# Kernel optimization log

Measured on AMD Instinct MI355X. Metric: run time of the kernel, lower is better.

Reference implementation:

```python
import jax, jax.numpy as jnp
import numpy as np

N_NODES = 50000
N_EDGES = 800000
IN_CH, HID_CH, OUT_CH = 128, 256, 128


def setup_inputs() -> dict:
    key = jax.random.key(0)
    k1, k2, k3, k4 = jax.random.split(key, 4)
    x = jax.random.normal(k1, (N_NODES, IN_CH), dtype=jnp.float32)
    edge_index = jax.random.randint(k2, (2, N_EDGES), 0, N_NODES, dtype=jnp.int32)
    # Glorot-ish scaled weights
    W1 = jax.random.normal(k3, (IN_CH, HID_CH), dtype=jnp.float32) * (1.0 / np.sqrt(IN_CH))
    b1 = jnp.zeros((HID_CH,), dtype=jnp.float32)
    W2 = jax.random.normal(k4, (HID_CH, OUT_CH), dtype=jnp.float32) * (1.0 / np.sqrt(HID_CH))
    b2 = jnpp = jnp.zeros((OUT_CH,), dtype=jnp.float32)
    return {"x": x, "edge_index": edge_index, "W1": W1, "b1": b1, "W2": W2, "b2": b2}


def _gcn_conv(x, W, b, src, dst, num_nodes):
    """PyG GCNConv: add self-loops, symmetric deg^-1/2 norm, linear, scatter-add."""
    h = x @ W  # [N, out] dense transform first (as in GCNConv)
    # in-degree including self-loops (edge weights = 1)
    deg = jax.ops.segment_sum(jnp.ones_like(dst, dtype=h.dtype), dst, num_segments=num_nodes)
    deg = deg + 1.0  # self-loop contribution
    dinv = jnp.where(deg > 0, jax.lax.rsqrt(deg), 0.0)
    # neighbor messages: norm_e * h[src_e], scatter-added to dst
    norm = dinv[src] * dinv[dst]                      # [E]
    msg = h[src] * norm[:, None]                      # [E, out] gather
    agg = jax.ops.segment_sum(msg, dst, num_segments=num_nodes)  # scatter-add
    # self-loop messages: dinv[i]^2 * h[i]
    agg = agg + h * (dinv * dinv)[:, None]
    return agg + b


def reference(x, edge_index, W1, b1, W2, b2):
    src, dst = edge_index[0], edge_index[1]
    n = x.shape[0]
    h = jax.nn.relu(_gcn_conv(x, W1, b1, src, dst, n))
    return _gcn_conv(h, W2, b2, src, dst, n)
```

## Files before the change

### kernel.cpp

```cpp
#include <hip/hip_runtime.h>

#define N_NODES 50000
#define N_EDGES 800000
#define IN_CH 128
#define HID_CH 256
#define OUT_CH 128
#define BUCKET 64

#define N_XCD 8
#define NODES_PER_XCD 6250

using half8 = __attribute__((ext_vector_type(8))) _Float16;
using f32x4 = __attribute__((ext_vector_type(4))) float;


#define FILL_CHUNKS 3125
#define FILL_BLOCKS (FILL_CHUNKS * N_XCD)
#define CVT_BLOCKS 3125
#define WT1_BLOCKS 256
#define WT2_BLOCKS 128

__global__ __launch_bounds__(256) void prep_kernel(const int* __restrict__ src,
                                                   const int* __restrict__ dst,
                                                   int* __restrict__ cnt,
                                                   unsigned short* __restrict__ bucket,
                                                   const float* __restrict__ x,
                                                   _Float16* __restrict__ x16,
                                                   const float* __restrict__ W1,
                                                   _Float16* __restrict__ W1T,
                                                   const float* __restrict__ W2,
                                                   _Float16* __restrict__ W2T) {
    int b = blockIdx.x, t = threadIdx.x;
    if (b < FILL_BLOCKS) {
        int g = b & 7;
        int chunk = b >> 3;
        int i = chunk * 256 + t;
        if (i < N_EDGES) {
            int d = dst[i];
            int lo = g * NODES_PER_XCD;
            if (d >= lo && d < lo + NODES_PER_XCD) {
                int s = src[i];
                int p = atomicAdd(&cnt[d], 1);
                if (p < BUCKET) bucket[(size_t)d * BUCKET + p] = (unsigned short)s;
            }
        }
    } else if (b < FILL_BLOCKS + CVT_BLOCKS) {
        int i = (b - FILL_BLOCKS) * 256 + t;
        float4 v0 = ((const float4*)x)[i * 2];
        float4 v1 = ((const float4*)x)[i * 2 + 1];
        half8 o = {(_Float16)v0.x, (_Float16)v0.y, (_Float16)v0.z, (_Float16)v0.w,
                   (_Float16)v1.x, (_Float16)v1.y, (_Float16)v1.z, (_Float16)v1.w};
        ((half8*)x16)[i] = o;
    } else if (b < FILL_BLOCKS + CVT_BLOCKS + WT1_BLOCKS) {
        int n = b - FILL_BLOCKS - CVT_BLOCKS;
        if (t < IN_CH) W1T[(size_t)n * IN_CH + t] = (_Float16)W1[(size_t)t * HID_CH + n];
    } else {
        int n = b - FILL_BLOCKS - CVT_BLOCKS - WT1_BLOCKS;
        if (t < HID_CH) W2T[(size_t)n * HID_CH + t] = (_Float16)W2[(size_t)t * OUT_CH + n];
    }
}


template <bool OUT16>
__global__ __launch_bounds__(256) void agg16_kernel(const _Float16* __restrict__ h16,
                                                    const int* __restrict__ cnt,
                                                    const unsigned short* __restrict__ bucket,
                                                    const float* __restrict__ bias,
                                                    void* __restrict__ outp) {
    int t = blockIdx.x * 256 + threadIdx.x;
    int v = t >> 4;
    int sub = t & 15;
    int deg = min(cnt[v], BUCKET);
    float dv = rsqrtf((float)cnt[v] + 1.0f);
    half8 hv = ((const half8*)(h16 + (size_t)v * 128))[sub];
    float acc[8];
#pragma unroll
    for (int i = 0; i < 8; i++) acc[i] = (float)hv[i] * dv * dv;

    const unsigned short* bk = bucket + (size_t)v * BUCKET;
    for (int base = 0; base < deg; base += 16) {
        int idx = base + sub;
        int a = 0;
        float c = 0.f;
        if (idx < deg) {
            a = bk[idx];
            c = rsqrtf((float)cnt[a] + 1.0f) * dv;
        }
        int len = min(deg - base, 16);
        int j = 0;
        for (; j + 8 <= len; j += 8) {
            int   s0 = __shfl(a, j + 0, 16); float w0 = __shfl(c, j + 0, 16);
            int   s1 = __shfl(a, j + 1, 16); float w1 = __shfl(c, j + 1, 16);
            int   s2 = __shfl(a, j + 2, 16); float w2 = __shfl(c, j + 2, 16);
            int   s3 = __shfl(a, j + 3, 16); float w3 = __shfl(c, j + 3, 16);
            int   s4 = __shfl(a, j + 4, 16); float w4 = __shfl(c, j + 4, 16);
            int   s5 = __shfl(a, j + 5, 16); float w5 = __shfl(c, j + 5, 16);
            int   s6 = __shfl(a, j + 6, 16); float w6 = __shfl(c, j + 6, 16);
            int   s7 = __shfl(a, j + 7, 16); float w7 = __shfl(c, j + 7, 16);
            half8 x0 = ((const half8*)(h16 + (size_t)s0 * 128))[sub];
            half8 x1 = ((const half8*)(h16 + (size_t)s1 * 128))[sub];
            half8 x2 = ((const half8*)(h16 + (size_t)s2 * 128))[sub];
            half8 x3 = ((const half8*)(h16 + (size_t)s3 * 128))[sub];
            half8 x4 = ((const half8*)(h16 + (size_t)s4 * 128))[sub];
            half8 x5 = ((const half8*)(h16 + (size_t)s5 * 128))[sub];
            half8 x6 = ((const half8*)(h16 + (size_t)s6 * 128))[sub];
            half8 x7 = ((const half8*)(h16 + (size_t)s7 * 128))[sub];
#pragma unroll
            for (int i = 0; i < 8; i++) acc[i] += w0 * (float)x0[i];
#pragma unroll
            for (int i = 0; i < 8; i++) acc[i] += w1 * (float)x1[i];
#pragma unroll
            for (int i = 0; i < 8; i++) acc[i] += w2 * (float)x2[i];
#pragma unroll
            for (int i = 0; i < 8; i++) acc[i] += w3 * (float)x3[i];
#pragma unroll
            for (int i = 0; i < 8; i++) acc[i] += w4 * (float)x4[i];
#pragma unroll
            for (int i = 0; i < 8; i++) acc[i] += w5 * (float)x5[i];
#pragma unroll
            for (int i = 0; i < 8; i++) acc[i] += w6 * (float)x6[i];
#pragma unroll
            for (int i = 0; i < 8; i++) acc[i] += w7 * (float)x7[i];
        }
        for (; j + 4 <= len; j += 4) {
            int   s0 = __shfl(a, j + 0, 16); float w0 = __shfl(c, j + 0, 16);
            int   s1 = __shfl(a, j + 1, 16); float w1 = __shfl(c, j + 1, 16);
            int   s2 = __shfl(a, j + 2, 16); float w2 = __shfl(c, j + 2, 16);
            int   s3 = __shfl(a, j + 3, 16); float w3 = __shfl(c, j + 3, 16);
            half8 x0 = ((const half8*)(h16 + (size_t)s0 * 128))[sub];
            half8 x1 = ((const half8*)(h16 + (size_t)s1 * 128))[sub];
            half8 x2 = ((const half8*)(h16 + (size_t)s2 * 128))[sub];
            half8 x3 = ((const half8*)(h16 + (size_t)s3 * 128))[sub];
#pragma unroll
            for (int i = 0; i < 8; i++) acc[i] += w0 * (float)x0[i];
#pragma unroll
            for (int i = 0; i < 8; i++) acc[i] += w1 * (float)x1[i];
#pragma unroll
            for (int i = 0; i < 8; i++) acc[i] += w2 * (float)x2[i];
#pragma unroll
            for (int i = 0; i < 8; i++) acc[i] += w3 * (float)x3[i];
        }
        for (; j < len; j++) {
            int   s = __shfl(a, j, 16);
            float w = __shfl(c, j, 16);
            half8 xv = ((const half8*)(h16 + (size_t)s * 128))[sub];
#pragma unroll
            for (int i = 0; i < 8; i++) acc[i] += w * (float)xv[i];
        }
    }

    if (OUT16) {
        half8 o;
#pragma unroll
        for (int i = 0; i < 8; i++) o[i] = (_Float16)acc[i];
        ((half8*)outp)[(size_t)v * 16 + sub] = o;
    } else {
        const float4* bp = (const float4*)bias;
        float4 b0 = bp[sub * 2], b1v = bp[sub * 2 + 1];
        float4 o0 = make_float4(acc[0] + b0.x, acc[1] + b0.y, acc[2] + b0.z, acc[3] + b0.w);
        float4 o1 = make_float4(acc[4] + b1v.x, acc[5] + b1v.y, acc[6] + b1v.z, acc[7] + b1v.w);
        float4* op = (float4*)outp;
        op[(size_t)v * 32 + sub * 2] = o0;
        op[(size_t)v * 32 + sub * 2 + 1] = o1;
    }
}


__global__ __launch_bounds__(256) void fused_mlp_kernel(const _Float16* __restrict__ A,
                                                        const _Float16* __restrict__ W1T,
                                                        const float* __restrict__ b1,
                                                        const _Float16* __restrict__ W2T,
                                                        _Float16* __restrict__ T2, int M) {
    const int LDH = 264;
    const int LDA = 136;
    const int LDB = 40;
    __shared__ __align__(16) _Float16 h1s[64 * LDH];
    __shared__ __align__(16) _Float16 As[64 * LDA];
    __shared__ __align__(16) _Float16 Bs[128 * LDB];

    int tid = threadIdx.x;
    int wave = tid >> 6, lane = tid & 63;
    int quad = lane >> 4, l16 = lane & 15;
    int wm = wave >> 1, wn = wave & 1;
    int bm = blockIdx.x * 64;

    for (int q = tid; q < 64 * 16; q += 256) {
        int row = q >> 4, seg = q & 15;
        int gr = bm + row;
        float4 v = make_float4(0.f, 0.f, 0.f, 0.f);
        if (gr < M) v = *(const float4*)(A + (size_t)gr * IN_CH + seg * 8);
        *(float4*)(As + row * LDA + seg * 8) = v;
    }

    for (int nh = 0; nh < 2; nh++) {
        f32x4 acc[2][4] = {};
        for (int k0 = 0; k0 < IN_CH; k0 += 32) {
            for (int q = tid; q < 512; q += 256) {
                int row = q >> 2, seg = q & 3;
                float4 v = *(const float4*)(W1T + (size_t)(nh * 128 + row) * IN_CH + k0 + seg * 8);
                *(float4*)(Bs + row * LDB + seg * 8) = v;
            }
            __syncthreads();
            half8 af[2], bf[4];
#pragma unroll
            for (int mt = 0; mt < 2; mt++)
                af[mt] = *(const half8*)(As + (wm * 32 + mt * 16 + l16) * LDA + k0 + quad * 8);
#pragma unroll
            for (int nt = 0; nt < 4; nt++)
                bf[nt] = *(const half8*)(Bs + (wn * 64 + nt * 16 + l16) * LDB + quad * 8);
#pragma unroll
            for (int mt = 0; mt < 2; mt++)
#pragma unroll
                for (int nt = 0; nt < 4; nt++)
                    acc[mt][nt] = __builtin_amdgcn_mfma_f32_16x16x32_f16(af[mt], bf[nt], acc[mt][nt], 0, 0, 0);
            __syncthreads();
        }
#pragma unroll
        for (int mt = 0; mt < 2; mt++)
#pragma unroll
            for (int nt = 0; nt < 4; nt++)
#pragma unroll
                for (int r = 0; r < 4; r++) {
                    int ml = wm * 32 + mt * 16 + quad * 4 + r;
                    int nl = wn * 64 + nt * 16 + l16;
                    float v = acc[mt][nt][r] + b1[nh * 128 + nl];
                    h1s[ml * LDH + nh * 128 + nl] = (_Float16)fmaxf(v, 0.f);
                }
    }

    f32x4 acc2[2][4] = {};
    for (int k0 = 0; k0 < HID_CH; k0 += 32) {
        for (int q = tid; q < 512; q += 256) {
            int row = q >> 2, seg = q & 3;
            float4 v = *(const float4*)(W2T + (size_t)row * HID_CH + k0 + seg * 8);
            *(float4*)(Bs + row * LDB + seg * 8) = v;
        }
        __syncthreads();
        half8 af[2], bf[4];
#pragma unroll
        for (int mt = 0; mt < 2; mt++)
            af[mt] = *(const half8*)(h1s + (wm * 32 + mt * 16 + l16) * LDH + k0 + quad * 8);
#pragma unroll
        for (int nt = 0; nt < 4; nt++)
            bf[nt] = *(const half8*)(Bs + (wn * 64 + nt * 16 + l16) * LDB + quad * 8);
#pragma unroll
        for (int mt = 0; mt < 2; mt++)
#pragma unroll
            for (int nt = 0; nt < 4; nt++)
                acc2[mt][nt] = __builtin_amdgcn_mfma_f32_16x16x32_f16(af[mt], bf[nt], acc2[mt][nt], 0, 0, 0);
        __syncthreads();
    }

    _Float16* Cs = As;
#pragma unroll
    for (int mt = 0; mt < 2; mt++)
#pragma unroll
        for (int nt = 0; nt < 4; nt++)
#pragma unroll
            for (int r = 0; r < 4; r++) {
                int ml = wm * 32 + mt * 16 + quad * 4 + r;
                int nl = wn * 64 + nt * 16 + l16;
                Cs[ml * LDA + nl] = (_Float16)acc2[mt][nt][r];
            }
    __syncthreads();
    for (int q = tid; q < 64 * 16; q += 256) {
        int row = q >> 4, seg = q & 15;
        int gr = bm + row;
        if (gr < M)
            *(float4*)(T2 + (size_t)gr * OUT_CH + seg * 8) = *(const float4*)(Cs + row * LDA + seg * 8);
    }
}


extern "C" void kernel_launch(void* const* d_in, const int* in_sizes, int n_in,
                              void* d_out, int out_size, void* d_ws, size_t ws_size,
                              hipStream_t stream) {
    const float* x  = (const float*)d_in[0];
    const int*   ei = (const int*)d_in[1];
    const int*   src = ei;
    const int*   dst = ei + N_EDGES;
    const float* W1 = (const float*)d_in[2];
    const float* b1 = (const float*)d_in[3];
    const float* W2 = (const float*)d_in[4];
    const float* b2 = (const float*)d_in[5];
    float* out = (float*)d_out;

    char* w = (char*)d_ws;
    auto alloc = [&](size_t bytes) -> void* {
        void* p = (void*)w;
        w += (bytes + 255) & ~(size_t)255;
        return p;
    };
    int*            cnt    = (int*)alloc((size_t)N_NODES * 4);
    unsigned short* bucket = (unsigned short*)alloc((size_t)N_NODES * BUCKET * 2);
    _Float16*       x16    = (_Float16*)alloc((size_t)N_NODES * IN_CH * 2);
    _Float16*       a1     = (_Float16*)alloc((size_t)N_NODES * IN_CH * 2);
    _Float16*       t2     = (_Float16*)alloc((size_t)N_NODES * OUT_CH * 2);
    _Float16*       W1T    = (_Float16*)alloc((size_t)IN_CH * HID_CH * 2);
    _Float16*       W2T    = (_Float16*)alloc((size_t)HID_CH * OUT_CH * 2);

    hipMemsetAsync(cnt, 0, (size_t)N_NODES * 4, stream);

    prep_kernel<<<FILL_BLOCKS + CVT_BLOCKS + WT1_BLOCKS + WT2_BLOCKS, 256, 0, stream>>>(
        src, dst, cnt, bucket, x, x16, W1, W1T, W2, W2T);

    agg16_kernel<true><<<N_NODES * 16 / 256, 256, 0, stream>>>(x16, cnt, bucket, nullptr, a1);
    fused_mlp_kernel<<<(N_NODES + 63) / 64, 256, 0, stream>>>(a1, W1T, b1, W2T, t2, N_NODES);
    agg16_kernel<false><<<N_NODES * 16 / 256, 256, 0, stream>>>(t2, cnt, bucket, b2, out);
}
```

Before: 217.5 us.

## Load MLP operand fragments directly from global memory, drop LDS staging

The fused MLP kernel no longer stages the input tile and weight tiles in shared memory. Each wave reads its A fragments and W1T/W2T fragments straight from global memory (weights come through L2), which removes most __syncthreads barriers. Shared memory use drops to only the hidden buffer, which can allow higher occupancy. The cost is redundant global weight loads across waves and blocks in exchange for fewer barriers and less LDS traffic.

```diff
diff --git a/kernel.cpp b/kernel.cpp
--- a/kernel.cpp
+++ b/kernel.cpp
@@ -172,11 +172,8 @@
                                                         const _Float16* __restrict__ W2T,
                                                         _Float16* __restrict__ T2, int M) {
     const int LDH = 264;
-    const int LDA = 136;
-    const int LDB = 40;
+    const int LDC = 136;
     __shared__ __align__(16) _Float16 h1s[64 * LDH];
-    __shared__ __align__(16) _Float16 As[64 * LDA];
-    __shared__ __align__(16) _Float16 Bs[128 * LDB];
 
     int tid = threadIdx.x;
     int wave = tid >> 6, lane = tid & 63;
@@ -184,74 +181,69 @@
     int wm = wave >> 1, wn = wave & 1;
     int bm = blockIdx.x * 64;
 
-    for (int q = tid; q < 64 * 16; q += 256) {
-        int row = q >> 4, seg = q & 15;
-        int gr = bm + row;
-        float4 v = make_float4(0.f, 0.f, 0.f, 0.f);
-        if (gr < M) v = *(const float4*)(A + (size_t)gr * IN_CH + seg * 8);
-        *(float4*)(As + row * LDA + seg * 8) = v;
-    }
-
+    half8 af[2][4];
+#pragma unroll
+    for (int mt = 0; mt < 2; mt++) {
+        int ar = bm + wm * 32 + mt * 16 + l16;
+        ar = min(ar, M - 1);
+#pragma unroll
+        for (int kq = 0; kq < 4; kq++)
+            af[mt][kq] = *(const half8*)(A + (size_t)ar * IN_CH + kq * 32 + quad * 8);
+    }
+
+#pragma unroll
     for (int nh = 0; nh < 2; nh++) {
         f32x4 acc[2][4] = {};
-        for (int k0 = 0; k0 < IN_CH; k0 += 32) {
-            for (int q = tid; q < 512; q += 256) {
-                int row = q >> 2, seg = q & 3;
-                float4 v = *(const float4*)(W1T + (size_t)(nh * 128 + row) * IN_CH + k0 + seg * 8);
-                *(float4*)(Bs + row * LDB + seg * 8) = v;
+#pragma unroll
+        for (int kq = 0; kq < 4; kq++) {
+            half8 bf[4];
+#pragma unroll
+            for (int nt = 0; nt < 4; nt++) {
+                int br = nh * 128 + wn * 64 + nt * 16 + l16;
+                bf[nt] = *(const half8*)(W1T + (size_t)br * IN_CH + kq * 32 + quad * 8);
             }
-            __syncthreads();
-            half8 af[2], bf[4];
 #pragma unroll
             for (int mt = 0; mt < 2; mt++)
-                af[mt] = *(const half8*)(As + (wm * 32 + mt * 16 + l16) * LDA + k0 + quad * 8);
-#pragma unroll
-            for (int nt = 0; nt < 4; nt++)
-                bf[nt] = *(const half8*)(Bs + (wn * 64 + nt * 16 + l16) * LDB + quad * 8);
+#pragma unroll
+                for (int nt = 0; nt < 4; nt++)
+                    acc[mt][nt] = __builtin_amdgcn_mfma_f32_16x16x32_f16(af[mt][kq], bf[nt], acc[mt][nt], 0, 0, 0);
+        }
+#pragma unroll
+        for (int nt = 0; nt < 4; nt++) {
+            int nl = wn * 64 + nt * 16 + l16;
+            float bb = b1[nh * 128 + nl];
 #pragma unroll
             for (int mt = 0; mt < 2; mt++)
-#pragma unroll
-                for (int nt = 0; nt < 4; nt++)
-                    acc[mt][nt] = __builtin_amdgcn_mfma_f32_16x16x32_f16(af[mt], bf[nt], acc[mt][nt], 0, 0, 0);
-            __syncthreads();
-        }
-#pragma unroll
-        for (int mt = 0; mt < 2; mt++)
-#pragma unroll
-            for (int nt = 0; nt < 4; nt++)
 #pragma unroll
                 for (int r = 0; r < 4; r++) {
                     int ml = wm * 32 + mt * 16 + quad * 4 + r;
-                    int nl = wn * 64 + nt * 16 + l16;
-                    float v = acc[mt][nt][r] + b1[nh * 128 + nl];
-                    h1s[ml * LDH + nh * 128 + nl] = (_Float16)fmaxf(v, 0.f);
+                    h1s[ml * LDH + nh * 128 + nl] = (_Float16)fmaxf(acc[mt][nt][r] + bb, 0.f);
                 }
-    }
+        }
+    }
+    __syncthreads();
 
     f32x4 acc2[2][4] = {};
-    for (int k0 = 0; k0 < HID_CH; k0 += 32) {
-        for (int q = tid; q < 512; q += 256) {
-            int row = q >> 2, seg = q & 3;
-            float4 v = *(const float4*)(W2T + (size_t)row * HID_CH + k0 + seg * 8);
-            *(float4*)(Bs + row * LDB + seg * 8) = v;
-        }
-        __syncthreads();
-        half8 af[2], bf[4];
+#pragma unroll
+    for (int kq = 0; kq < 8; kq++) {
+        half8 a2[2], bf[4];
 #pragma unroll
         for (int mt = 0; mt < 2; mt++)
-            af[mt] = *(const half8*)(h1s + (wm * 32 + mt * 16 + l16) * LDH + k0 + quad * 8);
-#pragma unroll
-        for (int nt = 0; nt < 4; nt++)
-            bf[nt] = *(const half8*)(Bs + (wn * 64 + nt * 16 + l16) * LDB + quad * 8);
+            a2[mt] = *(const half8*)(h1s + (wm * 32 + mt * 16 + l16) * LDH + kq * 32 + quad * 8);
+#pragma unroll
+        for (int nt = 0; nt < 4; nt++) {
+            int br = wn * 64 + nt * 16 + l16;
+            bf[nt] = *(const half8*)(W2T + (size_t)br * HID_CH + kq * 32 + quad * 8);
+        }
 #pragma unroll
         for (int mt = 0; mt < 2; mt++)
 #pragma unroll
             for (int nt = 0; nt < 4; nt++)
-                acc2[mt][nt] = __builtin_amdgcn_mfma_f32_16x16x32_f16(af[mt], bf[nt], acc2[mt][nt], 0, 0, 0);
-        __syncthreads();
-    }
-
-    _Float16* Cs = As;
+                acc2[mt][nt] = __builtin_amdgcn_mfma_f32_16x16x32_f16(a2[mt], bf[nt], acc2[mt][nt], 0, 0, 0);
+    }
+    __syncthreads();
+
+    _Float16* Cs = h1s;
 #pragma unroll
     for (int mt = 0; mt < 2; mt++)
 #pragma unroll
@@ -260,14 +252,14 @@
             for (int r = 0; r < 4; r++) {
                 int ml = wm * 32 + mt * 16 + quad * 4 + r;
                 int nl = wn * 64 + nt * 16 + l16;
-                Cs[ml * LDA + nl] = (_Float16)acc2[mt][nt][r];
+                Cs[ml * LDC + nl] = (_Float16)acc2[mt][nt][r];
             }
     __syncthreads();
     for (int q = tid; q < 64 * 16; q += 256) {
         int row = q >> 4, seg = q & 15;
         int gr = bm + row;
         if (gr < M)
-            *(float4*)(T2 + (size_t)gr * OUT_CH + seg * 8) = *(const float4*)(Cs + row * LDA + seg * 8);
+            *(float4*)(T2 + (size_t)gr * OUT_CH + seg * 8) = *(const float4*)(Cs + row * LDC + seg * 8);
     }
 }
 
```

Result: slower. 225.1 us (+3.5%).

## Build per-node edge buckets in shared memory with node-range partitioned blocks

Applied to the files above, without the earlier changes.

The edge bucketing is rebuilt so that each of 128 blocks owns a contiguous range of 391 destination nodes. Each block scans the full dst array with int4 loads, appends matching sources into a shared-memory bucket using shared atomics, and then copies counts and buckets to global memory in bulk. This removes global atomics and scattered global writes, and also drops the memset of the counts. In exchange every block rereads all 800K dst entries, only 128 blocks do this work, and each block needs about 50KB of LDS, which lowers occupancy for the whole fused prep kernel.

```diff
diff --git a/kernel.cpp b/kernel.cpp
--- a/kernel.cpp
+++ b/kernel.cpp
@@ -7,15 +7,12 @@
 #define OUT_CH 128
 #define BUCKET 64
 
-#define N_XCD 8
-#define NODES_PER_XCD 6250
-
 using half8 = __attribute__((ext_vector_type(8))) _Float16;
 using f32x4 = __attribute__((ext_vector_type(4))) float;
 
 
-#define FILL_CHUNKS 3125
-#define FILL_BLOCKS (FILL_CHUNKS * N_XCD)
+#define FILL_BLOCKS 128
+#define NODES_PER_FILL 391
 #define CVT_BLOCKS 3125
 #define WT1_BLOCKS 256
 #define WT2_BLOCKS 128
@@ -30,20 +27,44 @@
                                                    _Float16* __restrict__ W1T,
                                                    const float* __restrict__ W2,
                                                    _Float16* __restrict__ W2T) {
+    __shared__ int cnt_s[NODES_PER_FILL];
+    __shared__ unsigned short bucket_s[NODES_PER_FILL * BUCKET];
+
     int b = blockIdx.x, t = threadIdx.x;
     if (b < FILL_BLOCKS) {
-        int g = b & 7;
-        int chunk = b >> 3;
-        int i = chunk * 256 + t;
-        if (i < N_EDGES) {
-            int d = dst[i];
-            int lo = g * NODES_PER_XCD;
-            if (d >= lo && d < lo + NODES_PER_XCD) {
-                int s = src[i];
-                int p = atomicAdd(&cnt[d], 1);
-                if (p < BUCKET) bucket[(size_t)d * BUCKET + p] = (unsigned short)s;
-            }
-        }
+        int lo = b * NODES_PER_FILL;
+        int hi = min(lo + NODES_PER_FILL, N_NODES);
+        for (int i = t; i < NODES_PER_FILL; i += 256) cnt_s[i] = 0;
+        __syncthreads();
+
+        const int4* dst4 = (const int4*)dst;
+        for (int it = t; it < N_EDGES / 4; it += 256) {
+            int4 d4 = dst4[it];
+            int e = it * 4;
+            if (d4.x >= lo && d4.x < hi) {
+                int p = atomicAdd(&cnt_s[d4.x - lo], 1);
+                if (p < BUCKET) bucket_s[(d4.x - lo) * BUCKET + p] = (unsigned short)src[e + 0];
+            }
+            if (d4.y >= lo && d4.y < hi) {
+                int p = atomicAdd(&cnt_s[d4.y - lo], 1);
+                if (p < BUCKET) bucket_s[(d4.y - lo) * BUCKET + p] = (unsigned short)src[e + 1];
+            }
+            if (d4.z >= lo && d4.z < hi) {
+                int p = atomicAdd(&cnt_s[d4.z - lo], 1);
+                if (p < BUCKET) bucket_s[(d4.z - lo) * BUCKET + p] = (unsigned short)src[e + 2];
+            }
+            if (d4.w >= lo && d4.w < hi) {
+                int p = atomicAdd(&cnt_s[d4.w - lo], 1);
+                if (p < BUCKET) bucket_s[(d4.w - lo) * BUCKET + p] = (unsigned short)src[e + 3];
+            }
+        }
+        __syncthreads();
+
+        int nn = hi - lo;
+        for (int i = t; i < nn; i += 256) cnt[lo + i] = cnt_s[i];
+        int4* gb = (int4*)(bucket + (size_t)lo * BUCKET);
+        const int4* sb = (const int4*)bucket_s;
+        for (int i = t; i < nn * 8; i += 256) gb[i] = sb[i];
     } else if (b < FILL_BLOCKS + CVT_BLOCKS) {
         int i = (b - FILL_BLOCKS) * 256 + t;
         float4 v0 = ((const float4*)x)[i * 2];
@@ -292,15 +313,13 @@
         return p;
     };
     int*            cnt    = (int*)alloc((size_t)N_NODES * 4);
-    unsigned short* bucket = (unsigned short*)alloc((size_t)N_NODES * BUCKET * 2);
+    unsigned short* bucket = (unsigned short*)alloc((size_t)(FILL_BLOCKS * NODES_PER_FILL) * BUCKET * 2);
     _Float16*       x16    = (_Float16*)alloc((size_t)N_NODES * IN_CH * 2);
     _Float16*       a1     = (_Float16*)alloc((size_t)N_NODES * IN_CH * 2);
     _Float16*       t2     = (_Float16*)alloc((size_t)N_NODES * OUT_CH * 2);
     _Float16*       W1T    = (_Float16*)alloc((size_t)IN_CH * HID_CH * 2);
     _Float16*       W2T    = (_Float16*)alloc((size_t)HID_CH * OUT_CH * 2);
 
-    hipMemsetAsync(cnt, 0, (size_t)N_NODES * 4, stream);
-
     prep_kernel<<<FILL_BLOCKS + CVT_BLOCKS + WT1_BLOCKS + WT2_BLOCKS, 256, 0, stream>>>(
         src, dst, cnt, bucket, x, x16, W1, W1T, W2, W2T);
 
```

Result: slower. 638.2 us (+193.4%).
